# Optimization experiments

Hardware: AMD Instinct MI355X
Metric: run time of the kernel (lower is better)

The kernel has to match this reference:

```python
import jax, jax.numpy as jnp
import numpy as np

B, N, DIM = 16, 577, 768
HEADS, HEAD_DIM = 12, 64
QKV_DIM = HEADS * HEAD_DIM
MAX_REL = 14
TABLE_ROWS = 2 * MAX_REL + 2  # 30


def _rel_indices(n, max_rel):
    # Static (shape-only) 2D relative-position index matrices with CLS padding.
    m = n - 1
    side = int(m ** 0.5)
    r = np.arange(m)
    dv = r[None, :] // side - r[:, None] // side
    dh = r[None, :] % side - r[:, None] % side
    iv = np.clip(dv, -max_rel, max_rel) + max_rel + 1
    ih = np.clip(dh, -max_rel, max_rel) + max_rel + 1
    iv = np.pad(iv, ((1, 0), (1, 0)))  # CLS row/col -> index 0
    ih = np.pad(ih, ((1, 0), (1, 0)))
    return jnp.asarray(iv), jnp.asarray(ih)


def setup_inputs() -> dict:
    key = jax.random.key(0)
    ks = jax.random.split(key, 8)
    return {
        "x": jax.random.normal(ks[0], (B, N, DIM), jnp.float32),
        "qkv_w": jax.random.normal(ks[1], (3 * QKV_DIM, DIM), jnp.float32) * 0.02,
        "proj_w": jax.random.normal(ks[2], (DIM, QKV_DIM), jnp.float32) * 0.02,
        "proj_b": jnp.zeros((DIM,), jnp.float32),
        "tab_kv": jax.random.normal(ks[3], (TABLE_ROWS, HEAD_DIM), jnp.float32) * 0.02,
        "tab_kh": jax.random.normal(ks[4], (TABLE_ROWS, HEAD_DIM), jnp.float32) * 0.02,
        "tab_vv": jax.random.normal(ks[5], (TABLE_ROWS, HEAD_DIM), jnp.float32) * 0.02,
        "tab_vh": jax.random.normal(ks[6], (TABLE_ROWS, HEAD_DIM), jnp.float32) * 0.02,
    }


def reference(x, qkv_w, proj_w, proj_b, tab_kv, tab_kh, tab_vv, tab_vh):
    b, n, _ = x.shape
    scale = HEAD_DIM ** -0.5
    # qkv: [b,n,3*qkv_dim] -> [3,b,h,n,d]
    qkv = (x @ qkv_w.T).reshape(b, n, 3, HEADS, HEAD_DIM).transpose(2, 0, 3, 1, 4)
    q, k, v = qkv[0], qkv[1], qkv[2]
    attn = jnp.einsum('bhqd,bhkd->bhqk', q, k) * scale
    iv, ih = _rel_indices(n, MAX_REL)
    r_p_k = tab_kv[iv] + tab_kh[ih]  # [n,n,d]
    attn = attn + jnp.einsum('bhqd,qkd->bhqk', q, r_p_k) * scale
    attn = jax.nn.softmax(attn, axis=-1)
    out = jnp.einsum('bhqk,bhkd->bhqd', attn, v)
    r_p_v = tab_vv[iv] + tab_vh[ih]  # [n,n,d]
    out = out + jnp.einsum('bhqk,qkd->bhqd', attn, r_p_v)
    out = out.transpose(0, 2, 1, 3).reshape(b, n, QKV_DIM)
    return out @ proj_w.T + proj_b
```

## Files before the change

kernel.cpp:

```cpp
#include <hip/hip_runtime.h>


#define BB    16
#define NNq   577
#define DIMM  768
#define NHh   12
#define HD    64
#define MM    9232
#define QT    64
#define KT    64
#define NPAD  640
#define NW3   2304

typedef _Float16 h8 __attribute__((ext_vector_type(8)));
typedef _Float16 h4 __attribute__((ext_vector_type(4)));
typedef float    f4 __attribute__((ext_vector_type(4)));

__device__ inline h8 pack8(float4 a, float4 b) {
    h8 r;
    r[0]=(_Float16)a.x; r[1]=(_Float16)a.y; r[2]=(_Float16)a.z; r[3]=(_Float16)a.w;
    r[4]=(_Float16)b.x; r[5]=(_Float16)b.y; r[6]=(_Float16)b.z; r[7]=(_Float16)b.w;
    return r;
}

__global__ void init_all(const float* __restrict__ x, const float* __restrict__ w,
                         const float* __restrict__ pw,
                         _Float16* __restrict__ M2g, _Float16* __restrict__ vh,
                         _Float16* __restrict__ xh, _Float16* __restrict__ wh,
                         _Float16* __restrict__ pwh)
{
    const size_t id = (size_t)blockIdx.x*256 + threadIdx.x;
    if (id < NPAD*64) {
        const int key = (int)id >> 6, bin = (int)id & 63;
        int vb = 255, hb = 255;
        if (key == 0)      { vb = 24; hb = 49; }
        else if (key < NNq){ const int kq = key-1, kv = kq/24; vb = kv; hb = 25 + (kq - kv*24); }
        M2g[bin*NPAD + key] =
            ((key < NNq) && (bin==vb || bin==hb || bin==50)) ? (_Float16)1.f : (_Float16)0.f;
        return;
    }
    const size_t vid = id - NPAD*64;
    if (vid < (size_t)BB*NHh*HD*64) {
        const int head = (int)(vid >> 12);
        const int rem  = (int)vid & 4095;
        const int d    = rem >> 6;
        const int col  = 576 + (rem & 63);
        vh[(size_t)head*(HD*NPAD) + (size_t)d*NPAD + col] = (_Float16)0.f;
        return;
    }
    const size_t cid = vid - (size_t)BB*NHh*HD*64;
    const size_t NX = (size_t)MM*DIMM/4;
    const size_t NW = (size_t)NW3*DIMM/4;
    const size_t NP = (size_t)DIMM*DIMM/4;
    const float4* src; h4* dst; size_t j;
    if (cid < NX)            { src = (const float4*)x;  dst = (h4*)xh;  j = cid; }
    else if (cid < NX+NW)    { src = (const float4*)w;  dst = (h4*)wh;  j = cid - NX; }
    else if (cid < NX+NW+NP) { src = (const float4*)pw; dst = (h4*)pwh; j = cid - NX - NW; }
    else return;
    const float4 v = src[j];
    h4 hh; hh[0]=(_Float16)v.x; hh[1]=(_Float16)v.y; hh[2]=(_Float16)v.z; hh[3]=(_Float16)v.w;
    dst[j] = hh;
}

template <typename F>
__device__ __forceinline__ void gemm128f(const _Float16* __restrict__ Ah_g,
                                         const _Float16* __restrict__ Bh_g,
                                         F epi)
{
    __shared__ _Float16 Ah[128][40], Bh[128][40];
    const int t  = threadIdx.x;
    const int wv = t >> 6, lane = t & 63, lo = lane & 15, g = lane >> 4;
    const int wm = (wv >> 1) << 6, wn = (wv & 1) << 6;
    const int bm = blockIdx.y << 7, bn = blockIdx.x << 7;
    f4 acc[4][4] = {};
    const int lr = t >> 1;
    const int lc = (t & 1) << 4;
    const int am = bm + lr;
    const bool aok = am < MM;
    const _Float16* arh = Ah_g + (size_t)(aok ? am : 0) * DIMM + lc;
    const _Float16* brh = Bh_g + (size_t)(bn + lr) * DIMM + lc;

    for (int k0 = 0; k0 < DIMM; k0 += 32) {
        h8 a_h0 = {}, a_h1 = {};
        if (aok) {
            a_h0 = *(const h8*)(arh + k0); a_h1 = *(const h8*)(arh + k0 + 8);
        }
        const h8 b_h0 = *(const h8*)(brh + k0), b_h1 = *(const h8*)(brh + k0 + 8);
        __syncthreads();
        *(h8*)&Ah[lr][lc]   = a_h0;  *(h8*)&Ah[lr][lc+8] = a_h1;
        *(h8*)&Bh[lr][lc]   = b_h0;  *(h8*)&Bh[lr][lc+8] = b_h1;
        __syncthreads();
        h8 fah[4], fbh[4];
        #pragma unroll
        for (int i = 0; i < 4; ++i) {
            fah[i] = *(const h8*)&Ah[wm + 16*i + lo][g<<3];
            fbh[i] = *(const h8*)&Bh[wn + 16*i + lo][g<<3];
        }
        #pragma unroll
        for (int mi = 0; mi < 4; ++mi) {
            #pragma unroll
            for (int ni = 0; ni < 4; ++ni) {
                acc[mi][ni] = __builtin_amdgcn_mfma_f32_16x16x32_f16(fah[mi], fbh[ni], acc[mi][ni], 0, 0, 0);
            }
        }
    }
    epi(acc, bm, bn, wm, wn, lo, g);
}

__global__ __launch_bounds__(256, 3)
void qkv_gemm(const _Float16* __restrict__ xh, const _Float16* __restrict__ wh,
              _Float16* __restrict__ qh, _Float16* __restrict__ kh, _Float16* __restrict__ vh)
{
    gemm128f(xh, wh, [=](f4 (&acc)[4][4], int bm, int bn, int wm, int wn, int lo, int g) {
        const int three = bn / 768;
        const int cb    = bn - three * 768;
        #pragma unroll
        for (int mi = 0; mi < 4; ++mi) {
            #pragma unroll
            for (int reg = 0; reg < 4; ++reg) {
                const int m = bm + wm + 16*mi + 4*g + reg;
                if (m >= MM) continue;
                const int b_ = m / NNq;
                const int n_ = m - b_ * NNq;
                #pragma unroll
                for (int ni = 0; ni < 4; ++ni) {
                    const int n  = cb + wn + 16*ni + lo;
                    const int hh = n >> 6;
                    const int d  = n & 63;
                    if (three == 0) {
                        qh[((size_t)(b_*NHh + hh)*NPAD + n_)*HD + d] =
                            (_Float16)(acc[mi][ni][reg] * 0.18033688f);
                    } else if (three == 1) {
                        kh[((size_t)(b_*NHh + hh)*NPAD + n_)*HD + d] = (_Float16)acc[mi][ni][reg];
                    } else {
                        vh[((size_t)(b_*NHh + hh)*HD + d)*NPAD + n_] = (_Float16)acc[mi][ni][reg];
                    }
                }
            }
        }
    });
}

__global__ __launch_bounds__(256, 3)
void proj_gemm(const _Float16* __restrict__ aoh, const _Float16* __restrict__ pwh,
               const float* __restrict__ bias, float* __restrict__ out)
{
    gemm128f(aoh, pwh, [=](f4 (&acc)[4][4], int bm, int bn, int wm, int wn, int lo, int g) {
        #pragma unroll
        for (int ni = 0; ni < 4; ++ni) {
            const int n  = bn + wn + 16*ni + lo;
            const float bb = bias[n];
            #pragma unroll
            for (int mi = 0; mi < 4; ++mi) {
                #pragma unroll
                for (int reg = 0; reg < 4; ++reg) {
                    const int m = bm + wm + 16*mi + 4*g + reg;
                    if (m >= MM) continue;
                    out[(size_t)m*DIMM + n] = acc[mi][ni][reg] + bb;
                }
            }
        }
    });
}

__global__ __launch_bounds__(256, 2)
void attn_fused(const _Float16* __restrict__ qh,
                const _Float16* __restrict__ kh, const _Float16* __restrict__ vh,
                const float* __restrict__ tkv, const float* __restrict__ tkh,
                const float* __restrict__ tvv, const float* __restrict__ tvh,
                const _Float16* __restrict__ M2g,
                _Float16* __restrict__ aoh)
{
    __shared__ __align__(16) char smem[34048];
    _Float16 (*qrelS)[72] = (_Float16(*)[72])(smem);
    _Float16 (*Pt)[72]    = (_Float16(*)[72])(smem + 9216);
    float    (*TvS)[65]   = (float(*)[65])(smem + 18432);
    float    (*binsS)[52] = (float(*)[52])(smem);

    const int t    = threadIdx.x;
    const int w    = t >> 6;
    const int lane = t & 63;
    const int lo   = lane & 15;
    const int g    = lane >> 4;
    const int gb   = g << 3;

    const int blk = blockIdx.x;
    const int x8  = blk & 7;
    const int r_  = blk >> 3;
    const int hq  = r_ / 10;
    const int qt  = r_ - hq*10;
    const int bh  = x8 + (hq << 3);
    const int qt0 = qt * QT;
    const int qrow = 16*w + 4*g;
    const _Float16* qp = qh + (size_t)bh * (NPAD*HD);
    const _Float16* kp = kh + (size_t)bh * (NPAD*HD);
    const _Float16* vp = vh + (size_t)bh * (HD*NPAD);

    for (int e = t; e < 60*64; e += 256) {
        const int r = e >> 6, d = e & 63;
        TvS[r][d] = (r < 30) ? tvv[r*HD + d] : tvh[(r-30)*HD + d];
    }

    const h8 a0 = *(const h8*)(qp + (size_t)(qt0 + 16*w + lo)*HD + gb);
    const h8 a1 = *(const h8*)(qp + (size_t)(qt0 + 16*w + lo)*HD + 32 + gb);

    {
        f4 qacc[4] = {f4{0,0,0,0}, f4{0,0,0,0}, f4{0,0,0,0}, f4{0,0,0,0}};
        #pragma unroll
        for (int c = 0; c < 4; ++c) {
            const int r16 = 16*c + lo;
            const float* src = (r16 < 30) ? (tkv + r16*HD) : (tkh + (r16-30)*HD);
            h8 tb0 = {}, tb1 = {};
            if (r16 < 60) {
                tb0 = pack8(*(const float4*)(src + gb),      *(const float4*)(src + gb + 4));
                tb1 = pack8(*(const float4*)(src + 32 + gb), *(const float4*)(src + 32 + gb + 4));
            }
            qacc[c] = __builtin_amdgcn_mfma_f32_16x16x32_f16(a0, tb0, qacc[c], 0, 0, 0);
            qacc[c] = __builtin_amdgcn_mfma_f32_16x16x32_f16(a1, tb1, qacc[c], 0, 0, 0);
        }
        #pragma unroll
        for (int c = 0; c < 4; ++c) {
            #pragma unroll
            for (int i = 0; i < 4; ++i)
                qrelS[qrow + i][16*c + lo] = (_Float16)qacc[c][i];
        }
    }

    int qv_[4], qh_[4];
    bool q0_[4];
    #pragma unroll
    for (int i = 0; i < 4; ++i) {
        const int qgl = qt0 + qrow + i;
        q0_[i] = (qgl == 0);
        int qq = qgl - 1; if (qq < 0) qq = 0;
        qv_[i] = qq / 24;
        qh_[i] = qq - qv_[i]*24;
    }

    f4 o_acc [4] = {f4{0,0,0,0}, f4{0,0,0,0}, f4{0,0,0,0}, f4{0,0,0,0}};
    f4 binacc[4] = {f4{0,0,0,0}, f4{0,0,0,0}, f4{0,0,0,0}, f4{0,0,0,0}};

    for (int kt0 = 0; kt0 < 576; kt0 += KT) {
        h8 kb0[4], kb1[4], v0r[4], v1r[4], m20[4], m21[4];
        #pragma unroll
        for (int c = 0; c < 4; ++c) {
            const int key = kt0 + 16*c + lo;
            kb0[c] = *(const h8*)(kp + (size_t)key*HD + gb);
            kb1[c] = *(const h8*)(kp + (size_t)key*HD + 32 + gb);
            const int dd = 16*c + lo;
            v0r[c] = *(const h8*)(vp + (size_t)dd*NPAD + kt0 + gb);
            v1r[c] = *(const h8*)(vp + (size_t)dd*NPAD + kt0 + 32 + gb);
            m20[c] = *(const h8*)(M2g + (size_t)dd*NPAD + kt0 + gb);
            m21[c] = *(const h8*)(M2g + (size_t)dd*NPAD + kt0 + 32 + gb);
        }
        float srel[4][4];
        #pragma unroll
        for (int c = 0; c < 4; ++c) {
            const int key = kt0 + 16*c + lo;
            int kk = key - 1; if (kk < 0) kk = 0;
            const int kv  = kk / 24;
            const int kh2 = kk - kv*24;
            const bool kz = (key == 0);
            #pragma unroll
            for (int i = 0; i < 4; ++i) {
                int colv, colh;
                if (kz || q0_[i]) { colv = 0; colh = 30; }
                else {
                    int dv = kv  - qv_[i]; dv = min(14, max(-14, dv));
                    int dh = kh2 - qh_[i]; dh = min(14, max(-14, dh));
                    colv = dv + 15;
                    colh = 45 + dh;
                }
                srel[c][i] = (float)qrelS[qrow+i][colv] + (float)qrelS[qrow+i][colh];
            }
        }
        f4 Sc[4];
        #pragma unroll
        for (int c = 0; c < 4; ++c) {
            f4 acc = f4{0,0,0,0};
            acc = __builtin_amdgcn_mfma_f32_16x16x32_f16(a0, kb0[c], acc, 0, 0, 0);
            acc = __builtin_amdgcn_mfma_f32_16x16x32_f16(a1, kb1[c], acc, 0, 0, 0);
            Sc[c] = acc;
        }
        #pragma unroll
        for (int c = 0; c < 4; ++c) {
            #pragma unroll
            for (int i = 0; i < 4; ++i) {
                const float p = exp2f(Sc[c][i] + srel[c][i]);
                Pt[qrow+i][16*c + lo] = (_Float16)p;
            }
        }
        const h8 p0 = *(const h8*)&Pt[16*w + lo][gb];
        const h8 p1 = *(const h8*)&Pt[16*w + lo][32 + gb];
        #pragma unroll
        for (int c = 0; c < 4; ++c) {
            binacc[c] = __builtin_amdgcn_mfma_f32_16x16x32_f16(p0, m20[c], binacc[c], 0, 0, 0);
            binacc[c] = __builtin_amdgcn_mfma_f32_16x16x32_f16(p1, m21[c], binacc[c], 0, 0, 0);
        }
        #pragma unroll
        for (int c = 0; c < 4; ++c) {
            o_acc[c] = __builtin_amdgcn_mfma_f32_16x16x32_f16(p0, v0r[c], o_acc[c], 0, 0, 0);
            o_acc[c] = __builtin_amdgcn_mfma_f32_16x16x32_f16(p1, v1r[c], o_acc[c], 0, 0, 0);
        }
    }

    {
        const int kt0 = 576;
        h8 kb0_, kb1_, v0r[4], v1r[4], m20[4], m21[4];
        kb0_ = *(const h8*)(kp + (size_t)(kt0 + lo)*HD + gb);
        kb1_ = *(const h8*)(kp + (size_t)(kt0 + lo)*HD + 32 + gb);
        #pragma unroll
        for (int c = 0; c < 4; ++c) {
            const int dd = 16*c + lo;
            v0r[c] = *(const h8*)(vp + (size_t)dd*NPAD + kt0 + gb);
            v1r[c] = *(const h8*)(vp + (size_t)dd*NPAD + kt0 + 32 + gb);
            m20[c] = *(const h8*)(M2g + (size_t)dd*NPAD + kt0 + gb);
            m21[c] = *(const h8*)(M2g + (size_t)dd*NPAD + kt0 + 32 + gb);
        }
        float srel0[4];
        {
            const int key = kt0 + lo;
            int kk = key - 1; if (kk < 0) kk = 0;
            const int kv  = kk / 24;
            const int kh2 = kk - kv*24;
            #pragma unroll
            for (int i = 0; i < 4; ++i) {
                int colv, colh;
                if (q0_[i]) { colv = 0; colh = 30; }
                else {
                    int dv = kv  - qv_[i]; dv = min(14, max(-14, dv));
                    int dh = kh2 - qh_[i]; dh = min(14, max(-14, dh));
                    colv = dv + 15;
                    colh = 45 + dh;
                }
                srel0[i] = (float)qrelS[qrow+i][colv] + (float)qrelS[qrow+i][colh];
            }
        }
        f4 Sc0 = f4{0,0,0,0};
        Sc0 = __builtin_amdgcn_mfma_f32_16x16x32_f16(a0, kb0_, Sc0, 0, 0, 0);
        Sc0 = __builtin_amdgcn_mfma_f32_16x16x32_f16(a1, kb1_, Sc0, 0, 0, 0);
        {
            const bool ok = (kt0 + lo) < NNq;
            #pragma unroll
            for (int i = 0; i < 4; ++i) {
                const float p = ok ? exp2f(Sc0[i] + srel0[i]) : 0.f;
                Pt[qrow+i][lo] = (_Float16)p;
            }
            #pragma unroll
            for (int c = 1; c < 4; ++c) {
                #pragma unroll
                for (int i = 0; i < 4; ++i)
                    Pt[qrow+i][16*c + lo] = (_Float16)0.f;
            }
        }
        const h8 p0 = *(const h8*)&Pt[16*w + lo][gb];
        const h8 p1 = *(const h8*)&Pt[16*w + lo][32 + gb];
        #pragma unroll
        for (int c = 0; c < 4; ++c) {
            binacc[c] = __builtin_amdgcn_mfma_f32_16x16x32_f16(p0, m20[c], binacc[c], 0, 0, 0);
            binacc[c] = __builtin_amdgcn_mfma_f32_16x16x32_f16(p1, m21[c], binacc[c], 0, 0, 0);
        }
        #pragma unroll
        for (int c = 0; c < 4; ++c) {
            o_acc[c] = __builtin_amdgcn_mfma_f32_16x16x32_f16(p0, v0r[c], o_acc[c], 0, 0, 0);
            o_acc[c] = __builtin_amdgcn_mfma_f32_16x16x32_f16(p1, v1r[c], o_acc[c], 0, 0, 0);
        }
    }

    __syncthreads();
    #pragma unroll
    for (int c = 0; c < 4; ++c) {
        const int bc = 16*c + lo;
        if (bc <= 50) {
            #pragma unroll
            for (int i = 0; i < 4; ++i) binsS[qrow+i][bc] = binacc[c][i];
        }
    }
    __syncthreads();

    const int b_ = bh / NHh;
    const int h_ = bh - b_*NHh;
    #pragma unroll
    for (int i = 0; i < 4; ++i) {
        const int qr  = qrow + i;
        const int qgl = qt0 + qr;
        if (qgl >= NNq) continue;
        const float l    = binsS[qr][50];
        const float invl = 1.f / l;
        float o[4] = {o_acc[0][i], o_acc[1][i], o_acc[2][i], o_acc[3][i]};
        if (qgl == 0) {
            #pragma unroll
            for (int c = 0; c < 4; ++c) {
                const int d = 16*c + lo;
                o[c] += l * (TvS[0][d] + TvS[30][d]);
            }
        } else {
            #pragma unroll
            for (int bin = 0; bin < 24; ++bin) {
                const float wq = binsS[qr][bin];
                int dv = bin - qv_[i]; dv = min(14, max(-14, dv));
                #pragma unroll
                for (int c = 0; c < 4; ++c) o[c] += wq * TvS[dv+15][16*c + lo];
            }
            {
                const float wq = binsS[qr][24];
                #pragma unroll
                for (int c = 0; c < 4; ++c) o[c] += wq * TvS[0][16*c + lo];
            }
            #pragma unroll
            for (int bin = 0; bin < 24; ++bin) {
                const float wq = binsS[qr][25+bin];
                int dh = bin - qh_[i]; dh = min(14, max(-14, dh));
                #pragma unroll
                for (int c = 0; c < 4; ++c) o[c] += wq * TvS[45+dh][16*c + lo];
            }
            {
                const float wq = binsS[qr][49];
                #pragma unroll
                for (int c = 0; c < 4; ++c) o[c] += wq * TvS[30][16*c + lo];
            }
        }
        _Float16* dst = aoh + (size_t)(b_*NNq + qgl)*DIMM + h_*HD;
        #pragma unroll
        for (int c = 0; c < 4; ++c) dst[16*c + lo] = (_Float16)(o[c] * invl);
    }
}

extern "C" void kernel_launch(void* const* d_in, const int* in_sizes, int n_in,
                              void* d_out, int out_size, void* d_ws, size_t ws_size,
                              hipStream_t stream)
{
    const float* x      = (const float*)d_in[0];
    const float* qkv_w  = (const float*)d_in[1];
    const float* proj_w = (const float*)d_in[2];
    const float* proj_b = (const float*)d_in[3];
    const float* tkv    = (const float*)d_in[4];
    const float* tkh    = (const float*)d_in[5];
    const float* tvv    = (const float*)d_in[6];
    const float* tvh    = (const float*)d_in[7];
    float* out = (float*)d_out;
    float* ws  = (float*)d_ws;

    const size_t KV = (size_t)BB * NHh * NPAD * HD;
    _Float16* qh  = (_Float16*)ws;
    _Float16* kh  = qh + KV;
    _Float16* vh  = kh + KV;
    _Float16* aoh = vh + KV;
    _Float16* M2g = aoh + (size_t)MM*DIMM;
    _Float16* xh  = M2g + NPAD*64;
    _Float16* wh  = xh + (size_t)MM*DIMM;
    _Float16* pwh = wh + (size_t)NW3*DIMM;

    dim3 b256(256, 1, 1);
    init_all<<<12460, b256, 0, stream>>>(x, qkv_w, proj_w, M2g, vh, xh, wh, pwh);

    dim3 g1(NW3/128, (MM + 127)/128, 1);
    qkv_gemm<<<g1, b256, 0, stream>>>(xh, wh, qh, kh, vh);

    attn_fused<<<dim3(1920,1,1), b256, 0, stream>>>(qh, kh, vh, tkv, tkh, tvv, tvh, M2g, aoh);

    dim3 g3(DIMM/128, (MM + 127)/128, 1);
    proj_gemm<<<g3, b256, 0, stream>>>(aoh, pwh, proj_b, out);
}
```

Before: 440.9 us.

## Load GEMM MFMA fragments directly from global memory, bypassing LDS staging

Both the QKV and projection GEMMs stop staging A/B tiles in shared memory. Each lane now reads its MFMA fragments straight from global memory, which removes both __syncthreads per k-step and the LDS round trip. The cost is that each element is fetched several times across waves, and the loads are 16-byte pieces spread over many rows. Those loads depend on L2/L1 hits for reuse, and the launch bounds drop to 2 blocks per SM to allow more registers.

```diff
diff --git a/kernel.cpp b/kernel.cpp
--- a/kernel.cpp
+++ b/kernel.cpp
@@ -63,55 +63,51 @@
 }
 
 template <typename F>
-__device__ __forceinline__ void gemm128f(const _Float16* __restrict__ Ah_g,
+__device__ __forceinline__ void gemm128n(const _Float16* __restrict__ Ah_g,
                                          const _Float16* __restrict__ Bh_g,
                                          F epi)
 {
-    __shared__ _Float16 Ah[128][40], Bh[128][40];
     const int t  = threadIdx.x;
     const int wv = t >> 6, lane = t & 63, lo = lane & 15, g = lane >> 4;
     const int wm = (wv >> 1) << 6, wn = (wv & 1) << 6;
     const int bm = blockIdx.y << 7, bn = blockIdx.x << 7;
+    const int gb = g << 3;
     f4 acc[4][4] = {};
-    const int lr = t >> 1;
-    const int lc = (t & 1) << 4;
-    const int am = bm + lr;
-    const bool aok = am < MM;
-    const _Float16* arh = Ah_g + (size_t)(aok ? am : 0) * DIMM + lc;
-    const _Float16* brh = Bh_g + (size_t)(bn + lr) * DIMM + lc;
+
+    const _Float16* ap[4];
+    const _Float16* bp[4];
+    #pragma unroll
+    for (int mi = 0; mi < 4; ++mi) {
+        int am = bm + wm + 16*mi + lo;
+        if (am >= MM) am = MM - 1;
+        ap[mi] = Ah_g + (size_t)am * DIMM + gb;
+    }
+    #pragma unroll
+    for (int ni = 0; ni < 4; ++ni)
+        bp[ni] = Bh_g + (size_t)(bn + wn + 16*ni + lo) * DIMM + gb;
 
     for (int k0 = 0; k0 < DIMM; k0 += 32) {
-        h8 a_h0 = {}, a_h1 = {};
-        if (aok) {
-            a_h0 = *(const h8*)(arh + k0); a_h1 = *(const h8*)(arh + k0 + 8);
-        }
-        const h8 b_h0 = *(const h8*)(brh + k0), b_h1 = *(const h8*)(brh + k0 + 8);
-        __syncthreads();
-        *(h8*)&Ah[lr][lc]   = a_h0;  *(h8*)&Ah[lr][lc+8] = a_h1;
-        *(h8*)&Bh[lr][lc]   = b_h0;  *(h8*)&Bh[lr][lc+8] = b_h1;
-        __syncthreads();
-        h8 fah[4], fbh[4];
-        #pragma unroll
-        for (int i = 0; i < 4; ++i) {
-            fah[i] = *(const h8*)&Ah[wm + 16*i + lo][g<<3];
-            fbh[i] = *(const h8*)&Bh[wn + 16*i + lo][g<<3];
-        }
+        h8 af[4], bf[4];
+        #pragma unroll
+        for (int mi = 0; mi < 4; ++mi) af[mi] = *(const h8*)(ap[mi] + k0);
+        #pragma unroll
+        for (int ni = 0; ni < 4; ++ni) bf[ni] = *(const h8*)(bp[ni] + k0);
         #pragma unroll
         for (int mi = 0; mi < 4; ++mi) {
             #pragma unroll
             for (int ni = 0; ni < 4; ++ni) {
-                acc[mi][ni] = __builtin_amdgcn_mfma_f32_16x16x32_f16(fah[mi], fbh[ni], acc[mi][ni], 0, 0, 0);
+                acc[mi][ni] = __builtin_amdgcn_mfma_f32_16x16x32_f16(af[mi], bf[ni], acc[mi][ni], 0, 0, 0);
             }
         }
     }
     epi(acc, bm, bn, wm, wn, lo, g);
 }
 
-__global__ __launch_bounds__(256, 3)
+__global__ __launch_bounds__(256, 2)
 void qkv_gemm(const _Float16* __restrict__ xh, const _Float16* __restrict__ wh,
               _Float16* __restrict__ qh, _Float16* __restrict__ kh, _Float16* __restrict__ vh)
 {
-    gemm128f(xh, wh, [=](f4 (&acc)[4][4], int bm, int bn, int wm, int wn, int lo, int g) {
+    gemm128n(xh, wh, [=](f4 (&acc)[4][4], int bm, int bn, int wm, int wn, int lo, int g) {
         const int three = bn / 768;
         const int cb    = bn - three * 768;
         #pragma unroll
@@ -141,11 +137,11 @@
     });
 }
 
-__global__ __launch_bounds__(256, 3)
+__global__ __launch_bounds__(256, 2)
 void proj_gemm(const _Float16* __restrict__ aoh, const _Float16* __restrict__ pwh,
                const float* __restrict__ bias, float* __restrict__ out)
 {
-    gemm128f(aoh, pwh, [=](f4 (&acc)[4][4], int bm, int bn, int wm, int wn, int lo, int g) {
+    gemm128n(aoh, pwh, [=](f4 (&acc)[4][4], int bm, int bn, int wm, int wn, int lo, int g) {
         #pragma unroll
         for (int ni = 0; ni < 4; ++ni) {
             const int n  = bn + wn + 16*ni + lo;
```

After: 539.9 us. 1.22x slower.
